# Kernel optimization log

Hardware: AMD Instinct MI355X
Metric: run time of the kernel (lower is better)

Reference implementation:

```python
import jax, jax.numpy as jnp
import numpy as np
from jax import lax

KS = 3            # kernel_size
K = 32            # cluster_num
NB = 32           # num_base_kernels
HID = 64          # mlp_hidden_dim
COUT = 64         # out_channels
MAX_ITER = 20
TOL = 0.005


def _unfold3(x):
    # torch nn.Unfold(k=3, pad=1): output channel order is (c, kh, kw)
    b, c, h, w = x.shape
    xp = jnp.pad(x, ((0, 0), (0, 0), (1, 1), (1, 1)))
    cols = [xp[:, :, i:i + h, j:j + w] for i in range(KS) for j in range(KS)]
    p = jnp.stack(cols, axis=2)  # [B, C, 9, H, W]
    return p.reshape(b, c * KS * KS, h * w).transpose(0, 2, 1)  # [B, HW, C*9]


def _kmeans_single(key, sample):
    # sample: [N, D]. Lloyd iterations with early stop on total center shift.
    n, d = sample.shape
    centers0 = sample[jax.random.permutation(key, n)[:K]]

    def assign(centers):
        d2 = (jnp.sum(sample * sample, 1, keepdims=True)
              - 2.0 * (sample @ centers.T)
              + jnp.sum(centers * centers, 1))
        return jnp.argmin(d2, axis=1)

    def body(carry):
        i, centers, _ = carry
        a = assign(centers)
        oh = jax.nn.one_hot(a, K, dtype=sample.dtype)  # [N, K]
        counts = oh.sum(0)                             # [K]
        sums = oh.T @ sample                           # [K, D]
        new = jnp.where(counts[:, None] > 0,
                        sums / jnp.maximum(counts, 1.0)[:, None],
                        centers)
        shift = jnp.sum(jnp.linalg.norm(new - centers, axis=1))
        return (i + 1, new, shift)

    def cond(carry):
        i, _, shift = carry
        return jnp.logical_and(i < MAX_ITER, shift >= TOL * n)

    init = (jnp.int32(0), centers0, jnp.asarray(jnp.inf, sample.dtype))
    _, centers, _ = lax.while_loop(cond, body, init)
    return assign(centers)


def _kmeans(features):
    keys = jax.random.split(jax.random.key(42), features.shape[0])
    return jax.vmap(_kmeans_single)(keys, features)


def _mlp(x, w1, b1, w2, b2, w3, b3):
    h = jax.nn.relu(x @ w1 + b1)
    h = jax.nn.relu(h @ w2 + b2)
    return h @ w3 + b3


def setup_inputs() -> dict:
    key = jax.random.key(0)
    ks = jax.random.split(key, 16)
    B, C, H, W = 2, 32, 64, 64
    F = C * KS * KS
    fan = 1.0 / np.sqrt(F)
    fanh = 1.0 / np.sqrt(HID)
    return {
        'x': jax.random.normal(ks[0], (B, C, H, W), jnp.float32),
        'base_kernels': jax.random.normal(ks[1], (NB, F, COUT), jnp.float32) * np.sqrt(2.0 / F),
        'kg_w1': jax.random.normal(ks[2], (F, HID), jnp.float32) * fan,
        'kg_b1': jnp.zeros((HID,), jnp.float32),
        'kg_w2': jax.random.normal(ks[3], (HID, HID), jnp.float32) * fanh,
        'kg_b2': jnp.zeros((HID,), jnp.float32),
        'kg_w3': jax.random.normal(ks[4], (HID, NB), jnp.float32) * fanh,
        'kg_b3': jnp.zeros((NB,), jnp.float32),
        'bg_w1': jax.random.normal(ks[5], (F, HID), jnp.float32) * fan,
        'bg_b1': jnp.zeros((HID,), jnp.float32),
        'bg_w2': jax.random.normal(ks[6], (HID, HID), jnp.float32) * fanh,
        'bg_b2': jnp.zeros((HID,), jnp.float32),
        'bg_w3': jax.random.normal(ks[7], (HID, COUT), jnp.float32) * fanh,
        'bg_b3': jnp.zeros((COUT,), jnp.float32),
    }


def reference(x, base_kernels, kg_w1, kg_b1, kg_w2, kg_b2, kg_w3, kg_b3,
              bg_w1, bg_b1, bg_w2, bg_b2, bg_w3, bg_b3):
    B, C, H, W = x.shape
    patches = _unfold3(x)  # [B, P, F] with F = C*9
    P = patches.shape[1]
    # observation features: mean over kernel area per channel
    obs = patches.reshape(B, P, C, KS * KS).mean(-1)  # [B, P, C]
    idx = _kmeans(obs)  # [B, P] int cluster assignments

    # per-cluster centers of the full patch features (scatter-mean)
    oh = jax.nn.one_hot(idx, K, dtype=patches.dtype)          # [B, P, K]
    sums = jnp.einsum('bpk,bpf->bkf', oh, patches)            # [B, K, F]
    counts = jnp.maximum(oh.sum(1), 1.0)                      # [B, K]
    centers = sums / counts[:, :, None]                       # [B, K, F]

    # adaptive kernels = softmax-mixture of base kernels
    attn = jax.nn.softmax(_mlp(centers, kg_w1, kg_b1, kg_w2, kg_b2, kg_w3, kg_b3), axis=-1)  # [B,K,NB]
    kernels = jnp.einsum('bkn,nfc->bkfc', attn, base_kernels)  # [B, K, F, COUT]
    biases = _mlp(centers, bg_w1, bg_b1, bg_w2, bg_b2, bg_w3, bg_b3)  # [B, K, COUT]

    # combine: out[b,p] = patches[b,p] @ kernels[b, idx[b,p]] + biases[b, idx[b,p]]
    bidx = jnp.arange(B)[:, None]
    wtok = kernels[bidx, idx]   # [B, P, F, COUT]
    btok = biases[bidx, idx]    # [B, P, COUT]
    out = jnp.einsum('bpf,bpfc->bpc', patches, wtok) + btok
    out = out.transpose(0, 2, 1).reshape(B, COUT, H, W)
    return (out, idx)
```

## Files before the change

### kernel.cpp

```cpp
#include <hip/hip_runtime.h>
#include <hip/hip_bf16.h>
#include <vector>
#include <algorithm>
#include <utility>
#include <stdint.h>

#define BB 2
#define PP 4096
#define FF 288
#define KK 32
#define NBASE 32
#define HID 64
#define COUT 64
#define NWG_KM 32
#define SUBS 16
#define OUT_ELEMS 524288

#define THREEFRY_PARTITIONABLE 1

typedef unsigned short u16;

#define OFF_IDX    512
#define OFF_BIAS   41472
#define OFF_PART   57856
#define OFF_CNTS   320000
#define OFF_CPART  328192
#define OFF_WG     1544704
#define OFF_BAR2   3904000

struct InitIdx { int v[2][32]; };

__device__ __forceinline__ float bf2f(u16 u){
  union { unsigned int i; float f; } cv; cv.i = ((unsigned int)u) << 16; return cv.f;
}
__device__ __forceinline__ u16 f2bf(float f){
  union { float f; unsigned int i; } cv; cv.f = f;
  unsigned int x = cv.i;
  unsigned int r = (x + 0x7FFFu + ((x >> 16) & 1u)) >> 16;
  return (u16)r;
}
__device__ __forceinline__ float u_lo(unsigned int u){
  union { unsigned int i; float f; } cv; cv.i = u << 16; return cv.f;
}
__device__ __forceinline__ float u_hi(unsigned int u){
  union { unsigned int i; float f; } cv; cv.i = u & 0xFFFF0000u; return cv.f;
}

__device__ __forceinline__ void st_agent(float* p, float v){
  __hip_atomic_store(reinterpret_cast<unsigned int*>(p), __float_as_uint(v),
                     __ATOMIC_RELAXED, __HIP_MEMORY_SCOPE_AGENT);
}
__device__ __forceinline__ float ld_agent(const float* p){
  unsigned int u = __hip_atomic_load(reinterpret_cast<const unsigned int*>(p),
                                     __ATOMIC_RELAXED, __HIP_MEMORY_SCOPE_AGENT);
  return __uint_as_float(u);
}
__device__ __forceinline__ void st_agent_u32(unsigned int* p, unsigned int v){
  __hip_atomic_store(p, v, __ATOMIC_RELAXED, __HIP_MEMORY_SCOPE_AGENT);
}
__device__ __forceinline__ void st_slot(int* p, int v){
  __hip_atomic_store(p, v, __ATOMIC_RELAXED, __HIP_MEMORY_SCOPE_AGENT);
}
__device__ __forceinline__ int ld_slot(const int* p){
  return __hip_atomic_load(p, __ATOMIC_RELAXED, __HIP_MEMORY_SCOPE_AGENT);
}

template<bool BF>
__device__ __forceinline__ float ld(const void* p, size_t i){
  if constexpr (BF) { return bf2f(((const u16*)p)[i]); }
  else              { return ((const float*)p)[i]; }
}
template<bool BF>
__device__ __forceinline__ void st(void* p, size_t i, float v){
  if constexpr (BF) { ((u16*)p)[i] = f2bf(v); }
  else              { ((float*)p)[i] = v; }
}

__device__ __forceinline__ bool self_detect(const void* x, int* cntS){
  const int t = threadIdx.x, nb = blockDim.x;
  if (t == 0) *cntS = 0;
  __syncthreads();
  const u16* p = (const u16*)x;
  int bad = 0;
  for (int i = t; i < 1024; i += nb){
    u16 u = p[2*i];
    unsigned e = (u >> 7) & 0xFFu;
    if (e >= 131u) ++bad;
  }
  if (bad) atomicAdd(cntS, bad);
  __syncthreads();
  bool r = (*cntS < 102);
  __syncthreads();
  return r;
}

template<bool BF>
__device__ __forceinline__ float obs_chan(const void* x, size_t bi, int h, int w){
  float s = 0.f;
  #pragma unroll
  for (int dh=-1; dh<=1; ++dh){
    int hh = h + dh;
    #pragma unroll
    for (int dw=-1; dw<=1; ++dw){
      int ww = w + dw;
      float v = 0.f;
      if ((unsigned)hh < 64u && (unsigned)ww < 64u) v = ld<BF>(x, bi + (hh<<6) + ww);
      s += v;
    }
  }
  return s / 9.0f;
}

__device__ __forceinline__ void gbar16(int* slots, int mb, int sub, int epoch){
  asm volatile("s_waitcnt vmcnt(0)" ::: "memory");
  __syncthreads();
  const int t = threadIdx.x;
  if (t == 0) st_slot(&slots[(mb*16 + sub)*16], epoch);
  if (t < 16){
    while (ld_slot(&slots[(mb*16 + t)*16]) < epoch){}
  }
  __atomic_signal_fence(__ATOMIC_SEQ_CST);
  __syncthreads();
}

template<bool BF>
__device__ void kB_body(const void* __restrict__ x,
                        float* __restrict__ part,
                        float* __restrict__ cnts,
                        int* __restrict__ idxg,
                        void* __restrict__ dout,
                        int* __restrict__ slots,
                        const InitIdx& ii,
                        float* obs_st, float* cent, float* cc_s, int* a_loc,
                        float* sq, float* snorm, float* cntsh,
                        float* acc8, float* cnt8){
  const int t   = threadIdx.x;
  const int wg  = blockIdx.x;
  const int mb  = wg >> 4;
  const int sub = wg & 15;
  const int pg  = sub*256 + t;
  const int d   = t & 31, oct = t >> 5;

  float o[32];
  {
    int h = pg >> 6, w = pg & 63;
    size_t xb = (size_t)mb << 17;
    for (int c=0; c<32; ++c){
      float v = obs_chan<BF>(x, xb + ((size_t)c<<12), h, w);
      o[c] = v; obs_st[t*33 + c] = v;
    }
  }
  if (t < 32){
    int q = ii.v[mb][t];
    int qh = q >> 6, qw = q & 63;
    size_t xq = (size_t)mb << 17;
    for (int c=0; c<32; ++c) cent[t*32 + c] = obs_chan<BF>(x, xq + ((size_t)c<<12), qh, qw);
  }
  __syncthreads();

  float ss = 0.f;
  #pragma unroll
  for (int dd=0; dd<32; ++dd) ss = fmaf(o[dd], o[dd], ss);

  bool act = true;
  int parity = 0;

  for (int it=0; it<20 && act; ++it){
    if (t < 32){
      float s = 0.f;
      #pragma unroll
      for (int dd=0; dd<32; ++dd){ float v = cent[t*32 + dd]; s = fmaf(v,v,s); }
      cc_s[t] = s;
    }
    __syncthreads();
    float best = 3.0e38f; int bk = 0;
    for (int k=0; k<32; k+=4){
      const float4* c0 = (const float4*)&cent[(k  )*32];
      const float4* c1 = (const float4*)&cent[(k+1)*32];
      const float4* c2 = (const float4*)&cent[(k+2)*32];
      const float4* c3 = (const float4*)&cent[(k+3)*32];
      float dt0=0.f, dt1=0.f, dt2=0.f, dt3=0.f;
      #pragma unroll
      for (int q=0; q<8; ++q){
        float4 a0 = c0[q], a1 = c1[q], a2 = c2[q], a3 = c3[q];
        float o0 = o[q*4+0], o1 = o[q*4+1], o2 = o[q*4+2], o3 = o[q*4+3];
        dt0 = fmaf(o0,a0.x,dt0); dt0 = fmaf(o1,a0.y,dt0); dt0 = fmaf(o2,a0.z,dt0); dt0 = fmaf(o3,a0.w,dt0);
        dt1 = fmaf(o0,a1.x,dt1); dt1 = fmaf(o1,a1.y,dt1); dt1 = fmaf(o2,a1.z,dt1); dt1 = fmaf(o3,a1.w,dt1);
        dt2 = fmaf(o0,a2.x,dt2); dt2 = fmaf(o1,a2.y,dt2); dt2 = fmaf(o2,a2.z,dt2); dt2 = fmaf(o3,a2.w,dt2);
        dt3 = fmaf(o0,a3.x,dt3); dt3 = fmaf(o1,a3.y,dt3); dt3 = fmaf(o2,a3.z,dt3); dt3 = fmaf(o3,a3.w,dt3);
      }
      float di0 = (ss - 2.0f*dt0) + cc_s[k];
      float di1 = (ss - 2.0f*dt1) + cc_s[k+1];
      float di2 = (ss - 2.0f*dt2) + cc_s[k+2];
      float di3 = (ss - 2.0f*dt3) + cc_s[k+3];
      if (di0 < best){ best = di0; bk = k; }
      if (di1 < best){ best = di1; bk = k+1; }
      if (di2 < best){ best = di2; bk = k+2; }
      if (di3 < best){ best = di3; bk = k+3; }
    }
    a_loc[t] = bk;
    __syncthreads();
    for (int e=t; e<8*32*33; e+=256) acc8[e] = 0.f;
    cnt8[t] = 0.f;
    __syncthreads();
    {
      const int p0 = oct*32;
      int kcur = a_loc[p0];
      float racc = 0.f; int rl = 0;
      for (int i=0; i<32; ++i){
        int kp = a_loc[p0+i];
        float v = obs_st[(p0+i)*33 + d];
        if (kp != kcur){
          acc8[(oct*32 + kcur)*33 + d] += racc;
          if (d == 0) cnt8[oct*32 + kcur] += (float)rl;
          racc = 0.f; rl = 0; kcur = kp;
        }
        racc += v; ++rl;
      }
      acc8[(oct*32 + kcur)*33 + d] += racc;
      if (d == 0) cnt8[oct*32 + kcur] += (float)rl;
    }
    __syncthreads();
    float* Pg = part + ((size_t)((parity*2 + mb)*SUBS + sub))*1024;
    {
      float r0=0.f, r1=0.f, r2=0.f, r3=0.f;
      #pragma unroll
      for (int o2=0; o2<8; ++o2){
        r0 += acc8[(o2*32 + oct      )*33 + d];
        r1 += acc8[(o2*32 + oct + 8  )*33 + d];
        r2 += acc8[(o2*32 + oct + 16 )*33 + d];
        r3 += acc8[(o2*32 + oct + 24 )*33 + d];
      }
      st_agent(&Pg[(oct     )*32 + d], r0);
      st_agent(&Pg[(oct + 8 )*32 + d], r1);
      st_agent(&Pg[(oct + 16)*32 + d], r2);
      st_agent(&Pg[(oct + 24)*32 + d], r3);
    }
    if (t < 32){
      float c = 0.f;
      #pragma unroll
      for (int o2=0; o2<8; ++o2) c += cnt8[o2*32 + t];
      st_agent(&cnts[((size_t)((parity*2 + mb)*SUBS + sub))*32 + t], c);
    }
    gbar16(slots, mb, sub, it+1);
    {
      const float* Pb = part + (size_t)((parity*2 + mb)*SUBS)*1024;
      const float* Cb = cnts + (size_t)((parity*2 + mb)*SUBS)*32;
      if (t < 32){
        float s = 0.f;
        #pragma unroll
        for (int si=0; si<SUBS; ++si) s += ld_agent(&Cb[si*32 + t]);
        cntsh[t] = s;
      }
      __syncthreads();
      {
        int k = t >> 3, d4 = (t & 7) * 4;
        float vx = 0.f, vy = 0.f, vz = 0.f, vw = 0.f;
        #pragma unroll
        for (int si=0; si<SUBS; ++si){
          const float* pp = &Pb[si*1024 + k*32 + d4];
          float a0 = ld_agent(pp+0);
          float a1 = ld_agent(pp+1);
          float a2 = ld_agent(pp+2);
          float a3 = ld_agent(pp+3);
          vx += a0; vy += a1; vz += a2; vw += a3;
        }
        float cn = cntsh[k];
        float den = fmaxf(cn, 1.f);
        bool pos = cn > 0.f;
        float o0 = cent[k*32 + d4+0], o1 = cent[k*32 + d4+1];
        float o2 = cent[k*32 + d4+2], o3 = cent[k*32 + d4+3];
        float n0 = pos ? (vx / den) : o0;
        float n1 = pos ? (vy / den) : o1;
        float n2 = pos ? (vz / den) : o2;
        float n3 = pos ? (vw / den) : o3;
        float e0 = n0-o0, e1 = n1-o1, e2 = n2-o2, e3 = n3-o3;
        sq[k*32 + d4+0] = e0*e0; sq[k*32 + d4+1] = e1*e1;
        sq[k*32 + d4+2] = e2*e2; sq[k*32 + d4+3] = e3*e3;
        cent[k*32 + d4+0] = n0; cent[k*32 + d4+1] = n1;
        cent[k*32 + d4+2] = n2; cent[k*32 + d4+3] = n3;
      }
      __syncthreads();
      if (t < 32){
        float s = 0.f;
        #pragma unroll
        for (int dd=0; dd<32; ++dd) s += sq[t*32 + dd];
        snorm[t] = sqrtf(s);
      }
      __syncthreads();
      float sh = 0.f;
      for (int k=0;k<32;++k) sh += snorm[k];
      act = ((it+1) < 20) && ((double)sh >= 20.48);
      __syncthreads();
    }
    parity ^= 1;
  }
  if (t == 0) st_slot(&slots[(mb*16 + sub)*16], 0x7FFFFFFF);
  __syncthreads();
  if (t < 32){
    float s = 0.f;
    #pragma unroll
    for (int dd=0; dd<32; ++dd){ float v = cent[t*32 + dd]; s = fmaf(v,v,s); }
    cc_s[t] = s;
  }
  __syncthreads();
  float best = 3.0e38f; int bk = 0;
  for (int k=0; k<32; k+=4){
    const float4* c0 = (const float4*)&cent[(k  )*32];
    const float4* c1 = (const float4*)&cent[(k+1)*32];
    const float4* c2 = (const float4*)&cent[(k+2)*32];
    const float4* c3 = (const float4*)&cent[(k+3)*32];
    float dt0=0.f, dt1=0.f, dt2=0.f, dt3=0.f;
    #pragma unroll
    for (int q=0; q<8; ++q){
      float4 a0 = c0[q], a1 = c1[q], a2 = c2[q], a3 = c3[q];
      float o0 = o[q*4+0], o1 = o[q*4+1], o2 = o[q*4+2], o3 = o[q*4+3];
      dt0 = fmaf(o0,a0.x,dt0); dt0 = fmaf(o1,a0.y,dt0); dt0 = fmaf(o2,a0.z,dt0); dt0 = fmaf(o3,a0.w,dt0);
      dt1 = fmaf(o0,a1.x,dt1); dt1 = fmaf(o1,a1.y,dt1); dt1 = fmaf(o2,a1.z,dt1); dt1 = fmaf(o3,a1.w,dt1);
      dt2 = fmaf(o0,a2.x,dt2); dt2 = fmaf(o1,a2.y,dt2); dt2 = fmaf(o2,a2.z,dt2); dt2 = fmaf(o3,a2.w,dt2);
      dt3 = fmaf(o0,a3.x,dt3); dt3 = fmaf(o1,a3.y,dt3); dt3 = fmaf(o2,a3.z,dt3); dt3 = fmaf(o3,a3.w,dt3);
    }
    float di0 = (ss - 2.0f*dt0) + cc_s[k];
    float di1 = (ss - 2.0f*dt1) + cc_s[k+1];
    float di2 = (ss - 2.0f*dt2) + cc_s[k+2];
    float di3 = (ss - 2.0f*dt3) + cc_s[k+3];
    if (di0 < best){ best = di0; bk = k; }
    if (di1 < best){ best = di1; bk = k+1; }
    if (di2 < best){ best = di2; bk = k+2; }
    if (di3 < best){ best = di3; bk = k+3; }
  }
  idxg[mb*PP + pg] = bk;
  st<BF>(dout, (size_t)OUT_ELEMS + mb*PP + pg, (float)bk);
}

__global__ __launch_bounds__(256) void kB(const void* x, float* part, float* cnts,
                                          int* idxg, void* dout,
                                          int* slots, InitIdx ii){
  __shared__ __align__(16) float obs_st[256*33];
  __shared__ __align__(16) float cent[32*32];
  __shared__ float cc_s[32];
  __shared__ int   a_loc[256];
  __shared__ float sq[32*32];
  __shared__ float snorm[32];
  __shared__ float cntsh[32];
  __shared__ float acc8[8*32*33];
  __shared__ float cnt8[8*32];
  __shared__ int   cntS;
  if (self_detect(x, &cntS))
       kB_body<true >(x, part, cnts, idxg, dout, slots, ii,
                      obs_st, cent, cc_s, a_loc, sq, snorm, cntsh, acc8, cnt8);
  else kB_body<false>(x, part, cnts, idxg, dout, slots, ii,
                      obs_st, cent, cc_s, a_loc, sq, snorm, cntsh, acc8, cnt8);
}

template<bool BF>
__device__ void kC_item(int wgid, const void* __restrict__ x,
                        const int* __restrict__ idxg,
                        float* __restrict__ cpartJ,
                        float* __restrict__ tv,
                        int* __restrict__ idxsh,
                        float* __restrict__ acc8,
                        float* __restrict__ cnt8){
  int cg = wgid / 9, j = wgid % 9;
  int b = cg >> 4, pc = cg & 15;
  int t = threadIdx.x;
  const int d = t & 31, oct = t >> 5;

  idxsh[t] = idxg[b*PP + pc*256 + t];
  int dh = j/3 - 1, dw = j%3 - 1;
  for (int e=t; e<8192; e+=256){
    int c = e >> 8, p = e & 255;
    int gp = (pc << 8) + p;
    int h = gp >> 6, w = gp & 63;
    int hh = h + dh, ww = w + dw;
    float v = 0.f;
    if ((unsigned)hh < 64u && (unsigned)ww < 64u)
      v = ld<BF>(x, ((size_t)b << 17) + ((size_t)c << 12) + (hh<<6) + ww);
    tv[p*33 + c] = v;
  }
  for (int e=t; e<8*32*33; e+=256) acc8[e] = 0.f;
  cnt8[t] = 0.f;
  __syncthreads();
  {
    const int p0 = oct*32;
    int kcur = idxsh[p0];
    float racc = 0.f; int rl = 0;
    for (int i=0; i<32; ++i){
      int kp = idxsh[p0+i];
      float v = tv[(p0+i)*33 + d];
      if (kp != kcur){
        acc8[(oct*32 + kcur)*33 + d] += racc;
        if (d == 0) cnt8[oct*32 + kcur] += (float)rl;
        racc = 0.f; rl = 0; kcur = kp;
      }
      racc += v; ++rl;
    }
    acc8[(oct*32 + kcur)*33 + d] += racc;
    if (d == 0) cnt8[oct*32 + kcur] += (float)rl;
  }
  __syncthreads();
  float* cp = cpartJ + (size_t)wgid*(32*33);
  {
    float r0=0.f, r1=0.f, r2=0.f, r3=0.f;
    #pragma unroll
    for (int o2=0; o2<8; ++o2){
      r0 += acc8[(o2*32 + oct      )*33 + d];
      r1 += acc8[(o2*32 + oct + 8  )*33 + d];
      r2 += acc8[(o2*32 + oct + 16 )*33 + d];
      r3 += acc8[(o2*32 + oct + 24 )*33 + d];
    }
    st_agent(&cp[(oct     )*33 + d], r0);
    st_agent(&cp[(oct + 8 )*33 + d], r1);
    st_agent(&cp[(oct + 16)*33 + d], r2);
    st_agent(&cp[(oct + 24)*33 + d], r3);
  }
  if (j == 0 && t < 32){
    float c8 = 0.f;
    #pragma unroll
    for (int o2=0; o2<8; ++o2) c8 += cnt8[o2*32 + t];
    st_agent(&cp[t*33 + 32], c8);
  }
}

template<bool BF>
__device__ void kDE_item(int wg, const void* __restrict__ base,
                         const float* __restrict__ cpartJ,
                         const void* kg_w1, const void* kg_b1,
                         const void* kg_w2, const void* kg_b2,
                         const void* kg_w3, const void* kg_b3,
                         const void* bg_w1, const void* bg_b1,
                         const void* bg_w2, const void* bg_b2,
                         const void* bg_w3, const void* bg_b3,
                         float* __restrict__ biasO,
                         u16* __restrict__ Wg,
                         float* row, float* h1, float* h2, float* lgs,
                         float* at, float* tile){
  int fq = wg & 3, bk = wg >> 2;
  int b = bk >> 5, k = bk & 31;
  int t = threadIdx.x;

  if (t < 64){
    float cnt = 0.f;
    for (int ch=0; ch<16; ++ch)
      cnt += cpartJ[(size_t)((b*16+ch)*9)*(32*33) + k*33 + 32];
    float den = fmaxf(cnt, 1.f);
    for (int f=t; f<FF; f+=64){
      int c = f / 9, j = f % 9;
      float s = 0.f;
      for (int ch=0; ch<16; ++ch)
        s += cpartJ[(size_t)((b*16+ch)*9 + j)*(32*33) + k*33 + c];
      row[f] = s / den;
    }
  }
  __syncthreads();
  if (t < 64){
    float s = 0.f;
    #pragma unroll 8
    for (int f=0; f<FF; ++f) s = fmaf(row[f], ld<BF>(kg_w1, f*HID + t), s);
    h1[t] = fmaxf(s + ld<BF>(kg_b1, t), 0.f);
  }
  __syncthreads();
  if (t < 64){
    float s = 0.f;
    #pragma unroll 8
    for (int h=0; h<HID; ++h) s = fmaf(h1[h], ld<BF>(kg_w2, h*HID + t), s);
    h2[t] = fmaxf(s + ld<BF>(kg_b2, t), 0.f);
  }
  __syncthreads();
  if (t < 32){
    float s = 0.f;
    #pragma unroll 8
    for (int h=0; h<HID; ++h) s = fmaf(h2[h], ld<BF>(kg_w3, h*NBASE + t), s);
    lgs[t] = s + ld<BF>(kg_b3, t);
  }
  __syncthreads();
  if (t < 32){
    float mx = -3.0e38f;
    for (int i=0;i<NBASE;++i) mx = fmaxf(mx, lgs[i]);
    float se = 0.f;
    for (int i=0;i<NBASE;++i) se += expf(lgs[i]-mx);
    at[t] = expf(lgs[t]-mx) / se;
  }
  __syncthreads();
  if (t < 64){
    float s = 0.f;
    #pragma unroll 8
    for (int f=0; f<FF; ++f) s = fmaf(row[f], ld<BF>(bg_w1, f*HID + t), s);
    h1[t] = fmaxf(s + ld<BF>(bg_b1, t), 0.f);
  }
  __syncthreads();
  if (t < 64){
    float s = 0.f;
    #pragma unroll 8
    for (int h=0; h<HID; ++h) s = fmaf(h1[h], ld<BF>(bg_w2, h*HID + t), s);
    h2[t] = fmaxf(s + ld<BF>(bg_b2, t), 0.f);
  }
  __syncthreads();
  if (t < 64 && fq == 0){
    float s = 0.f;
    #pragma unroll 8
    for (int h=0; h<HID; ++h) s = fmaf(h2[h], ld<BF>(bg_w3, h*COUT + t), s);
    st_agent(&biasO[bk*COUT + t], s + ld<BF>(bg_b3, t));
  }
  __syncthreads();

  int f0 = fq*72;
  for (int e8 = t; e8 < 72*8; e8 += 256){
    int fl = e8 >> 3, cg = (e8 & 7) << 3;
    float s0=0.f,s1=0.f,s2=0.f,s3=0.f,s4=0.f,s5=0.f,s6=0.f,s7=0.f;
    if constexpr (BF){
      const u16* bp = (const u16*)base + (size_t)(f0 + fl)*COUT + cg;
      #pragma unroll 4
      for (int n=0; n<NBASE; ++n){
        uint4 v = *(const uint4*)(bp + (size_t)n*FF*COUT);
        float a = at[n];
        s0 = fmaf(a, u_lo(v.x), s0); s1 = fmaf(a, u_hi(v.x), s1);
        s2 = fmaf(a, u_lo(v.y), s2); s3 = fmaf(a, u_hi(v.y), s3);
        s4 = fmaf(a, u_lo(v.z), s4); s5 = fmaf(a, u_hi(v.z), s5);
        s6 = fmaf(a, u_lo(v.w), s6); s7 = fmaf(a, u_hi(v.w), s7);
      }
    } else {
      const float* bp = (const float*)base + (size_t)(f0 + fl)*COUT + cg;
      #pragma unroll 4
      for (int n=0; n<NBASE; ++n){
        float4 v0 = *(const float4*)(bp + (size_t)n*FF*COUT);
        float4 v1 = *(const float4*)(bp + (size_t)n*FF*COUT + 4);
        float a = at[n];
        s0 = fmaf(a, v0.x, s0); s1 = fmaf(a, v0.y, s1);
        s2 = fmaf(a, v0.z, s2); s3 = fmaf(a, v0.w, s3);
        s4 = fmaf(a, v1.x, s4); s5 = fmaf(a, v1.y, s5);
        s6 = fmaf(a, v1.z, s6); s7 = fmaf(a, v1.w, s7);
      }
    }
    float* tp = &tile[fl*65 + cg];
    tp[0]=s0; tp[1]=s1; tp[2]=s2; tp[3]=s3;
    tp[4]=s4; tp[5]=s5; tp[6]=s6; tp[7]=s7;
  }
  __syncthreads();
  for (int e=t; e<72*32; e+=256){
    int c = e / 36, fp = (e % 36) * 2;
    unsigned lo = f2bf(tile[(fp  )*65 + c]);
    unsigned hi = f2bf(tile[(fp+1)*65 + c]);
    unsigned* wp = (unsigned*)(Wg + (size_t)bk*(64*FF) + (size_t)c*FF + f0 + fp);
    st_agent_u32(wp, lo | (hi << 16));
  }
}

template<bool BF>
__device__ void kF_item(int item, const void* __restrict__ x,
                        const int* __restrict__ idxg,
                        const u16* __restrict__ Wg,
                        const float* __restrict__ biasO,
                        void* __restrict__ dout,
                        const int* __restrict__ wgflag,
                        u16* __restrict__ patch,
                        float* __restrict__ outT){
  int q = item & 3, h = (item >> 2) & 63, b = item >> 8;
  int t = threadIdx.x, wv = t >> 6, lane = t & 63;
  int w0 = q << 4;

  if (t < 16){
    int kk = idxg[(b << 12) + (h << 6) + w0 + t];
    while (ld_slot(&wgflag[(b << 5) + kk]) < 4) __builtin_amdgcn_s_sleep(8);
  }
  __syncthreads();

  for (int e=t; e<16*FF; e+=256){
    int pl = e & 15, fe = e >> 4;
    int c = fe / 9, j = fe % 9;
    int hh = h + j/3 - 1, ww = w0 + pl + (j%3) - 1;
    float v = 0.f;
    if ((unsigned)hh < 64u && (unsigned)ww < 64u)
      v = ld<BF>(x, ((size_t)b << 17) + ((size_t)c << 12) + (hh<<6) + ww);
    patch[pl*296 + fe] = f2bf(v);
  }
  __syncthreads();

  #pragma unroll
  for (int i=0; i<4; ++i){
    int pl = (wv << 2) + i;
    int p = (h << 6) + w0 + pl;
    int k = idxg[(b << 12) + p];
    const uint4* Wp = (const uint4*)(Wg + ((size_t)((b << 5) + k)*64 + lane)*FF);
    const uint4* Pp = (const uint4*)(patch + pl*296);
    float acc = 0.f;
    #pragma unroll 6
    for (int j=0; j<36; ++j){
      uint4 wv4 = Wp[j];
      uint4 pv4 = Pp[j];
      acc = fmaf(u_lo(pv4.x), u_lo(wv4.x), acc);
      acc = fmaf(u_hi(pv4.x), u_hi(wv4.x), acc);
      acc = fmaf(u_lo(pv4.y), u_lo(wv4.y), acc);
      acc = fmaf(u_hi(pv4.y), u_hi(wv4.y), acc);
      acc = fmaf(u_lo(pv4.z), u_lo(wv4.z), acc);
      acc = fmaf(u_hi(pv4.z), u_hi(wv4.z), acc);
      acc = fmaf(u_lo(pv4.w), u_lo(wv4.w), acc);
      acc = fmaf(u_hi(pv4.w), u_hi(wv4.w), acc);
    }
    float bias = biasO[((b << 5) + k)*COUT + lane];
    outT[lane*17 + pl] = acc + bias;
  }
  __syncthreads();

  for (int e=t; e<1024; e+=256){
    int cout = e >> 4, pl = e & 15;
    st<BF>(dout, (((size_t)(b << 6) + cout) << 12) + (h << 6) + w0 + pl,
           outT[cout*17 + pl]);
  }
}

template<bool BF>
__device__ void kCDEF_body(const void* x, const void* base,
                           const int* idxg, float* cpartJ,
                           const void* kg_w1, const void* kg_b1,
                           const void* kg_w2, const void* kg_b2,
                           const void* kg_w3, const void* kg_b3,
                           const void* bg_w1, const void* bg_b1,
                           const void* bg_w2, const void* bg_b2,
                           const void* bg_w3, const void* bg_b3,
                           float* biasO, u16* Wg, void* dout,
                           int* flags, char* sm){
  const int wg = blockIdx.x, t = threadIdx.x;
  int* cntC   = flags;
  int* wgflag = flags + 16;

  if (wg < 288){
    kC_item<BF>(wg, x, idxg, cpartJ,
                (float*)(sm + 0), (int*)(sm + 67584),
                (float*)(sm + 33792), (float*)(sm + 68608));
    asm volatile("s_waitcnt vmcnt(0)" ::: "memory");
    __syncthreads();
    if (t == 0) atomicAdd(cntC, 1);
  }

  if (wg < 256){
    if (t == 0){
      while (ld_slot(cntC) < 288) __builtin_amdgcn_s_sleep(8);
    }
    __syncthreads();
    kDE_item<BF>(wg, base, cpartJ, kg_w1,kg_b1,kg_w2,kg_b2,kg_w3,kg_b3,
                 bg_w1,bg_b1,bg_w2,bg_b2,bg_w3,bg_b3, biasO, Wg,
                 (float*)(sm + 0), (float*)(sm + 1152), (float*)(sm + 1408),
                 (float*)(sm + 1664), (float*)(sm + 1792), (float*)(sm + 1920));
    asm volatile("s_waitcnt vmcnt(0)" ::: "memory");
    __syncthreads();
    if (t == 0) atomicAdd(&wgflag[wg >> 2], 1);
  }
  __syncthreads();

  kF_item<BF>(wg, x, idxg, Wg, biasO, dout, wgflag,
              (u16*)(sm + 0), (float*)(sm + 9472));
}

__global__ __launch_bounds__(256) void kCDEF(const void* x, const void* base,
                           const int* idxg, float* cpartJ,
                           const void* kg_w1, const void* kg_b1,
                           const void* kg_w2, const void* kg_b2,
                           const void* kg_w3, const void* kg_b3,
                           const void* bg_w1, const void* bg_b1,
                           const void* bg_w2, const void* bg_b2,
                           const void* bg_w3, const void* bg_b3,
                           float* biasO, u16* Wg, void* dout, int* flags){
  __shared__ __align__(16) char sm[69632];
  __shared__ int cntS;
  if (self_detect(x, &cntS))
       kCDEF_body<true >(x, base, idxg, cpartJ,
                         kg_w1,kg_b1,kg_w2,kg_b2,kg_w3,kg_b3,
                         bg_w1,bg_b1,bg_w2,bg_b2,bg_w3,bg_b3,
                         biasO, Wg, dout, flags, sm);
  else kCDEF_body<false>(x, base, idxg, cpartJ,
                         kg_w1,kg_b1,kg_w2,kg_b2,kg_w3,kg_b3,
                         bg_w1,bg_b1,bg_w2,bg_b2,bg_w3,bg_b3,
                         biasO, Wg, dout, flags, sm);
}

static inline uint32_t rotl32(uint32_t x, int d){ return (x<<d)|(x>>(32-d)); }
static void tf_block(uint32_t k0,uint32_t k1,uint32_t x0,uint32_t x1,uint32_t&o0,uint32_t&o1){
  uint32_t ks2 = k0 ^ k1 ^ 0x1BD11BDAu;
  uint32_t v0 = x0 + k0, v1 = x1 + k1;
  const int ra[4]={13,15,26,6}, rb[4]={17,29,16,24};
  #define R4(r) for(int i_=0;i_<4;++i_){ v0 += v1; v1 = rotl32(v1,(r)[i_]); v1 ^= v0; }
  R4(ra); v0 += k1;  v1 += ks2 + 1u;
  R4(rb); v0 += ks2; v1 += k0  + 2u;
  R4(ra); v0 += k0;  v1 += k1  + 3u;
  R4(rb); v0 += k1;  v1 += ks2 + 4u;
  R4(ra); v0 += ks2; v1 += k0  + 5u;
  #undef R4
  o0 = v0; o1 = v1;
}
struct KP{ uint32_t a, b; };
static void tf_split(KP k, KP& first, KP& second){
#if THREEFRY_PARTITIONABLE
  uint32_t a0,b0,a1,b1;
  tf_block(k.a,k.b, 0u,0u, a0,b0);
  tf_block(k.a,k.b, 0u,1u, a1,b1);
  first  = KP{a0,b0};
  second = KP{a1,b1};
#else
  uint32_t a0,b0,a1,b1;
  tf_block(k.a,k.b, 0u,2u, a0,b0);
  tf_block(k.a,k.b, 1u,3u, a1,b1);
  first  = KP{a0,a1};
  second = KP{b0,b1};
#endif
}
static void random_bits_4096(KP k, std::vector<uint32_t>& bits){
#if THREEFRY_PARTITIONABLE
  for (int i=0;i<4096;++i){
    uint32_t o0,o1; tf_block(k.a,k.b, 0u,(uint32_t)i, o0,o1);
    bits[i] = o0 ^ o1;
  }
#else
  for (int i=0;i<2048;++i){
    uint32_t o0,o1; tf_block(k.a,k.b,(uint32_t)i,(uint32_t)(i+2048),o0,o1);
    bits[i] = o0; bits[i+2048] = o1;
  }
#endif
}
static void perm_first32(KP key, int* out32){
  std::vector<int> vals(4096);
  for (int i=0;i<4096;++i) vals[i] = i;
  std::vector<uint32_t> bits(4096);
  std::vector<std::pair<uint32_t,int>> pr(4096);
  KP k = key;
  for (int r=0;r<2;++r){
    KP nk, sk; tf_split(k, nk, sk); k = nk;
    random_bits_4096(sk, bits);
    for (int i=0;i<4096;++i) pr[i] = std::make_pair(bits[i], vals[i]);
    std::stable_sort(pr.begin(), pr.end(),
        [](const std::pair<uint32_t,int>& a, const std::pair<uint32_t,int>& c){ return a.first < c.first; });
    for (int i=0;i<4096;++i) vals[i] = pr[i].second;
  }
  for (int j=0;j<32;++j) out32[j] = vals[j];
}

static const InitIdx& get_init_idx(){
  static const InitIdx ii = [](){
    InitIdx r;
    KP root = KP{0u, 42u};
    KP kb0, kb1; tf_split(root, kb0, kb1);
    perm_first32(kb0, r.v[0]);
    perm_first32(kb1, r.v[1]);
    return r;
  }();
  return ii;
}

extern "C" void kernel_launch(void* const* d_in, const int* in_sizes, int n_in,
                              void* d_out, int out_size, void* d_ws, size_t ws_size,
                              hipStream_t stream) {
  const void* x     = d_in[0];
  const void* base  = d_in[1];
  const void* kg_w1 = d_in[2];
  const void* kg_b1 = d_in[3];
  const void* kg_w2 = d_in[4];
  const void* kg_b2 = d_in[5];
  const void* kg_w3 = d_in[6];
  const void* kg_b3 = d_in[7];
  const void* bg_w1 = d_in[8];
  const void* bg_b1 = d_in[9];
  const void* bg_w2 = d_in[10];
  const void* bg_b2 = d_in[11];
  const void* bg_w3 = d_in[12];
  const void* bg_b3 = d_in[13];

  char* ws = (char*)d_ws;
  int*   idxg  = (int*)(ws + OFF_IDX);
  float* biasO = (float*)(ws + OFF_BIAS);
  float* part  = (float*)(ws + OFF_PART);
  float* cnts  = (float*)(ws + OFF_CNTS);
  float* cpartJ= (float*)(ws + OFF_CPART);
  u16*   Wg    = (u16*)(ws + OFF_WG);
  int*   slots = (int*)(ws + OFF_BAR2);
  int*   flags = (int*)(ws + OFF_BAR2 + 2048);

  const InitIdx& ii = get_init_idx();

  hipMemsetAsync(ws + OFF_BAR2, 0, 3072, stream);
  kB<<<NWG_KM, 256, 0, stream>>>(x, part, cnts, idxg, d_out, slots, ii);
  kCDEF<<<512, 256, 0, stream>>>(x, base, idxg, cpartJ,
                                 kg_w1, kg_b1, kg_w2, kg_b2, kg_w3, kg_b3,
                                 bg_w1, bg_b1, bg_w2, bg_b2, bg_w3, bg_b3,
                                 biasO, Wg, d_out, flags);
}
```

Baseline: 274.0 us.

## Split cluster-center pass into its own kernel, drop in-kernel spin barrier

Moves the per-cluster partial-sum stage out of the fused kCDEF kernel into a separate kC launch with 288 workgroups. The spin-wait on a global counter and the agent-scope stores are replaced by the kernel boundary. The remaining kDEF kernel uses much less LDS (about 20 KB instead of about 68 KB), which should allow more workgroups per CU. The cost is an extra launch and the loss of overlap between the two stages.

```diff
diff --git a/kernel.cpp b/kernel.cpp
--- a/kernel.cpp
+++ b/kernel.cpp
@@ -354,13 +354,14 @@
 }
 
 template<bool BF>
-__device__ void kC_item(int wgid, const void* __restrict__ x,
+__device__ void kC_body(const void* __restrict__ x,
                         const int* __restrict__ idxg,
                         float* __restrict__ cpartJ,
                         float* __restrict__ tv,
                         int* __restrict__ idxsh,
                         float* __restrict__ acc8,
                         float* __restrict__ cnt8){
+  int wgid = blockIdx.x;
   int cg = wgid / 9, j = wgid % 9;
   int b = cg >> 4, pc = cg & 15;
   int t = threadIdx.x;
@@ -409,17 +410,28 @@
       r2 += acc8[(o2*32 + oct + 16 )*33 + d];
       r3 += acc8[(o2*32 + oct + 24 )*33 + d];
     }
-    st_agent(&cp[(oct     )*33 + d], r0);
-    st_agent(&cp[(oct + 8 )*33 + d], r1);
-    st_agent(&cp[(oct + 16)*33 + d], r2);
-    st_agent(&cp[(oct + 24)*33 + d], r3);
+    cp[(oct     )*33 + d] = r0;
+    cp[(oct + 8 )*33 + d] = r1;
+    cp[(oct + 16)*33 + d] = r2;
+    cp[(oct + 24)*33 + d] = r3;
   }
   if (j == 0 && t < 32){
     float c8 = 0.f;
     #pragma unroll
     for (int o2=0; o2<8; ++o2) c8 += cnt8[o2*32 + t];
-    st_agent(&cp[t*33 + 32], c8);
-  }
+    cp[t*33 + 32] = c8;
+  }
+}
+
+__global__ __launch_bounds__(256) void kC(const void* x, const int* idxg,
+                                          float* cpartJ){
+  __shared__ __align__(16) float tv[256*33];
+  __shared__ int   idxsh[256];
+  __shared__ __align__(16) float acc8[8*32*33];
+  __shared__ float cnt8[256];
+  __shared__ int   cntS;
+  if (self_detect(x, &cntS)) kC_body<true >(x, idxg, cpartJ, tv, idxsh, acc8, cnt8);
+  else                       kC_body<false>(x, idxg, cpartJ, tv, idxsh, acc8, cnt8);
 }
 
 template<bool BF>
@@ -610,34 +622,19 @@
 }
 
 template<bool BF>
-__device__ void kCDEF_body(const void* x, const void* base,
-                           const int* idxg, float* cpartJ,
-                           const void* kg_w1, const void* kg_b1,
-                           const void* kg_w2, const void* kg_b2,
-                           const void* kg_w3, const void* kg_b3,
-                           const void* bg_w1, const void* bg_b1,
-                           const void* bg_w2, const void* bg_b2,
-                           const void* bg_w3, const void* bg_b3,
-                           float* biasO, u16* Wg, void* dout,
-                           int* flags, char* sm){
+__device__ void kDEF_body(const void* x, const void* base,
+                          const int* idxg, const float* cpartJ,
+                          const void* kg_w1, const void* kg_b1,
+                          const void* kg_w2, const void* kg_b2,
+                          const void* kg_w3, const void* kg_b3,
+                          const void* bg_w1, const void* bg_b1,
+                          const void* bg_w2, const void* bg_b2,
+                          const void* bg_w3, const void* bg_b3,
+                          float* biasO, u16* Wg, void* dout,
+                          int* wgflag, char* sm){
   const int wg = blockIdx.x, t = threadIdx.x;
-  int* cntC   = flags;
-  int* wgflag = flags + 16;
-
-  if (wg < 288){
-    kC_item<BF>(wg, x, idxg, cpartJ,
-                (float*)(sm + 0), (int*)(sm + 67584),
-                (float*)(sm + 33792), (float*)(sm + 68608));
-    asm volatile("s_waitcnt vmcnt(0)" ::: "memory");
-    __syncthreads();
-    if (t == 0) atomicAdd(cntC, 1);
-  }
 
   if (wg < 256){
-    if (t == 0){
-      while (ld_slot(cntC) < 288) __builtin_amdgcn_s_sleep(8);
-    }
-    __syncthreads();
     kDE_item<BF>(wg, base, cpartJ, kg_w1,kg_b1,kg_w2,kg_b2,kg_w3,kg_b3,
                  bg_w1,bg_b1,bg_w2,bg_b2,bg_w3,bg_b3, biasO, Wg,
                  (float*)(sm + 0), (float*)(sm + 1152), (float*)(sm + 1408),
@@ -645,33 +642,33 @@
     asm volatile("s_waitcnt vmcnt(0)" ::: "memory");
     __syncthreads();
     if (t == 0) atomicAdd(&wgflag[wg >> 2], 1);
-  }
-  __syncthreads();
+    __syncthreads();
+  }
 
   kF_item<BF>(wg, x, idxg, Wg, biasO, dout, wgflag,
               (u16*)(sm + 0), (float*)(sm + 9472));
 }
 
-__global__ __launch_bounds__(256) void kCDEF(const void* x, const void* base,
-                           const int* idxg, float* cpartJ,
-                           const void* kg_w1, const void* kg_b1,
-                           const void* kg_w2, const void* kg_b2,
-                           const void* kg_w3, const void* kg_b3,
-                           const void* bg_w1, const void* bg_b1,
-                           const void* bg_w2, const void* bg_b2,
-                           const void* bg_w3, const void* bg_b3,
-                           float* biasO, u16* Wg, void* dout, int* flags){
-  __shared__ __align__(16) char sm[69632];
+__global__ __launch_bounds__(256) void kDEF(const void* x, const void* base,
+                          const int* idxg, const float* cpartJ,
+                          const void* kg_w1, const void* kg_b1,
+                          const void* kg_w2, const void* kg_b2,
+                          const void* kg_w3, const void* kg_b3,
+                          const void* bg_w1, const void* bg_b1,
+                          const void* bg_w2, const void* bg_b2,
+                          const void* bg_w3, const void* bg_b3,
+                          float* biasO, u16* Wg, void* dout, int* wgflag){
+  __shared__ __align__(16) char sm[20736];
   __shared__ int cntS;
   if (self_detect(x, &cntS))
-       kCDEF_body<true >(x, base, idxg, cpartJ,
-                         kg_w1,kg_b1,kg_w2,kg_b2,kg_w3,kg_b3,
-                         bg_w1,bg_b1,bg_w2,bg_b2,bg_w3,bg_b3,
-                         biasO, Wg, dout, flags, sm);
-  else kCDEF_body<false>(x, base, idxg, cpartJ,
-                         kg_w1,kg_b1,kg_w2,kg_b2,kg_w3,kg_b3,
-                         bg_w1,bg_b1,bg_w2,bg_b2,bg_w3,bg_b3,
-                         biasO, Wg, dout, flags, sm);
+       kDEF_body<true >(x, base, idxg, cpartJ,
+                        kg_w1,kg_b1,kg_w2,kg_b2,kg_w3,kg_b3,
+                        bg_w1,bg_b1,bg_w2,bg_b2,bg_w3,bg_b3,
+                        biasO, Wg, dout, wgflag, sm);
+  else kDEF_body<false>(x, base, idxg, cpartJ,
+                        kg_w1,kg_b1,kg_w2,kg_b2,kg_w3,kg_b3,
+                        bg_w1,bg_b1,bg_w2,bg_b2,bg_w3,bg_b3,
+                        biasO, Wg, dout, wgflag, sm);
 }
 
 static inline uint32_t rotl32(uint32_t x, int d){ return (x<<d)|(x>>(32-d)); }
@@ -772,14 +769,15 @@
   float* cpartJ= (float*)(ws + OFF_CPART);
   u16*   Wg    = (u16*)(ws + OFF_WG);
   int*   slots = (int*)(ws + OFF_BAR2);
-  int*   flags = (int*)(ws + OFF_BAR2 + 2048);
+  int*   wgflag= (int*)(ws + OFF_BAR2 + 2048);
 
   const InitIdx& ii = get_init_idx();
 
   hipMemsetAsync(ws + OFF_BAR2, 0, 3072, stream);
   kB<<<NWG_KM, 256, 0, stream>>>(x, part, cnts, idxg, d_out, slots, ii);
-  kCDEF<<<512, 256, 0, stream>>>(x, base, idxg, cpartJ,
-                                 kg_w1, kg_b1, kg_w2, kg_b2, kg_w3, kg_b3,
-                                 bg_w1, bg_b1, bg_w2, bg_b2, bg_w3, bg_b3,
-                                 biasO, Wg, d_out, flags);
-}
+  kC<<<288, 256, 0, stream>>>(x, idxg, cpartJ);
+  kDEF<<<512, 256, 0, stream>>>(x, base, idxg, cpartJ,
+                                kg_w1, kg_b1, kg_w2, kg_b2, kg_w3, kg_b3,
+                                bg_w1, bg_b1, bg_w2, bg_b2, bg_w3, bg_b3,
+                                biasO, Wg, d_out, wgflag);
+}
```

Result: faster. 268.0 us (-2.2%).
